# Kernel optimization log

Hardware: AMD Instinct MI355X
Metric: run time of the kernel (lower is better)

## Reference

```python
import jax, jax.numpy as jnp
import numpy as np

INPUT_DIM = 1024
OUTPUT_DIM = 1024
DEGREE = 8


def pentanacci_basis(x, degree):
    # x: [B, I] (already sigmoided). Returns [B, I, degree+1].
    # P0 = 0, P1 = 1, P2 = x, P3 = x, P4 = x^2,
    # Pn = x*P(n-1) + P(n-2) + P(n-3) + P(n-4) + P(n-5) for n >= 5
    zeros = jnp.zeros_like(x)
    ones = jnp.ones_like(x)
    seeds = [zeros, ones, x, x, x * x]
    basis = seeds[: degree + 1]
    for n in range(5, degree + 1):
        basis.append(x * basis[n - 1] + basis[n - 2] + basis[n - 3]
                     + basis[n - 4] + basis[n - 5])
    return jnp.stack(basis, axis=-1)


def setup_inputs() -> dict:
    key = jax.random.key(0)
    kx, kw = jax.random.split(key)
    x = jax.random.normal(kx, (4096, INPUT_DIM), dtype=jnp.float32)
    std = 1.0 / (INPUT_DIM * (DEGREE + 1))
    coeffs = std * jax.random.normal(kw, (INPUT_DIM, OUTPUT_DIM, DEGREE + 1),
                                     dtype=jnp.float32)
    return {"x": x, "coeffs": coeffs}


def reference(x, coeffs):
    degree = coeffs.shape[-1] - 1
    xs = jax.nn.sigmoid(x)                      # [B, I]
    basis = pentanacci_basis(xs, degree)        # [B, I, D+1]
    y = jnp.einsum('bid,iod->bo', basis, coeffs)  # [B, O]
    return y
```

## Files before the change

kernel.cpp:

```cpp
#include <hip/hip_runtime.h>
#include <stdint.h>

#define M_DIM 4096
#define I_DIM 1024
#define O_DIM 1024
#define KB 6
#define K_DIM (I_DIM * KB)
#define SPLITS 4

typedef __attribute__((ext_vector_type(8))) short short8;
typedef __attribute__((ext_vector_type(4))) float f32x4;
typedef __attribute__((ext_vector_type(4))) unsigned int u32x4;
typedef __attribute__((ext_vector_type(4))) float hfloat4;
typedef __attribute__((ext_vector_type(8))) _Float16 h16x8;

__device__ __forceinline__ unsigned short f2bf(float f) {
  union { float f; unsigned int u; } v; v.f = f;
  unsigned int u = v.u;
  unsigned int r = (u + 0x7FFFu + ((u >> 16) & 1u)) >> 16;
  return (unsigned short)r;
}

__global__ __launch_bounds__(256) void k_prep(const float* __restrict__ x,
                                              const float* __restrict__ C,
                                              unsigned short* __restrict__ A,
                                              unsigned short* __restrict__ Bt,
                                              float* __restrict__ partB) {
  const int bid = blockIdx.x;
  if (bid < 2048) {
    int t = bid * 256 + threadIdx.x;
    long e0 = (long)t * 8;
    const hfloat4* xp = (const hfloat4*)(x + e0);
    hfloat4 v0 = xp[0], v1 = xp[1];
    float xv[8];
    xv[0]=v0[0]; xv[1]=v0[1]; xv[2]=v0[2]; xv[3]=v0[3];
    xv[4]=v1[0]; xv[5]=v1[1]; xv[6]=v1[2]; xv[7]=v1[3];
    unsigned short outv[48];
#pragma unroll
    for (int e = 0; e < 8; ++e) {
      float s  = 1.0f / (1.0f + __expf(-xv[e]));
      float b2 = s, b3 = s, b4 = s * s;
      float b5 = fmaf(s, b4, b3 + b2 + 1.0f);
      float b6 = fmaf(s, b5, b4 + b3 + b2 + 1.0f);
      float b7 = fmaf(s, b6, b5 + b4 + b3 + b2);
      float b8 = fmaf(s, b7, b6 + b5 + b4 + b3);
      outv[e*6+0] = f2bf(s);
      outv[e*6+1] = f2bf(b4);
      outv[e*6+2] = f2bf(b5);
      outv[e*6+3] = f2bf(b6);
      outv[e*6+4] = f2bf(b7);
      outv[e*6+5] = f2bf(b8);
    }
    u32x4* dst = (u32x4*)(A + e0 * KB);
    const u32x4* srcv = (const u32x4*)outv;
#pragma unroll
    for (int q = 0; q < 6; ++q) dst[q] = srcv[q];
  } else {
    __shared__ unsigned short tile[32 * 192];
    __shared__ float bred[256];
    int b = bid - 2048;
    int i0 = (b & 31) * 32, o0 = (b >> 5) * 32;
    int t = threadIdx.x;
    int ol = t & 31, ig = t >> 5;
    float bsum = 0.f;
#pragma unroll
    for (int r = 0; r < 4; ++r) {
      int il = ig + r * 8;
      const float* p = C + (size_t)(i0 + il) * (O_DIM * 9) + (size_t)(o0 + ol) * 9;
      float c1 = p[1];
      float c2 = p[2], c3 = p[3], c4 = p[4], c5 = p[5], c6 = p[6], c7 = p[7], c8 = p[8];
      bsum += c1;
      unsigned short* q = &tile[ol * 192 + il * 6];
      q[0] = f2bf(c2 + c3);
      q[1] = f2bf(c4);
      q[2] = f2bf(c5);
      q[3] = f2bf(c6);
      q[4] = f2bf(c7);
      q[5] = f2bf(c8);
    }
    bred[t] = bsum;
    __syncthreads();
    if (t < 32) {
      float s = 0.f;
#pragma unroll
      for (int g = 0; g < 8; ++g) s += bred[g * 32 + t];
      partB[(size_t)(b & 31) * O_DIM + o0 + t] = s;
    }
    const u32x4* lsrc = (const u32x4*)tile;
#pragma unroll
    for (int r = 0; r < 3; ++r) {
      int c = t + r * 256;
      int row = c / 24, off = c % 24;
      u32x4* gdst = (u32x4*)(Bt + (size_t)(o0 + row) * K_DIM + (size_t)i0 * 6 + off * 8);
      *gdst = lsrc[c];
    }
  }
}

__global__ __launch_bounds__(256) void k_bias2(const float* __restrict__ partB,
                                               float* __restrict__ bias) {
  int o = blockIdx.x * 256 + threadIdx.x;
  float s = 0.f;
#pragma unroll
  for (int ib = 0; ib < 32; ++ib) s += partB[(size_t)ib * O_DIM + o];
  bias[o] = s;
}

#define SBAR __builtin_amdgcn_sched_barrier(0)

template<bool SPLIT>
__global__ __launch_bounds__(512, 2) void k_gemm8(const unsigned short* __restrict__ A,
                                                  const unsigned short* __restrict__ B,
                                                  const float* __restrict__ bias,
                                                  void* __restrict__ dst) {
  constexpr int CK = SPLIT ? (K_DIM / SPLITS) : K_DIM;
  constexpr int NT = CK / 64;
  constexpr int PPX = SPLIT ? 8 : 2;
  __shared__ char lds[131072];
  const int tid = threadIdx.x;
  const int lane = tid & 63, wid = tid >> 6;
  const int wm = wid >> 2, wn = wid & 3;
  const int l15 = lane & 15, lk = lane >> 4, l7 = lane & 7;
  const int flat = blockIdx.x + (blockIdx.y << 2) + (blockIdx.z << 6);
  const int xcd = flat & 7, slot = flat >> 3;
  const int panel = xcd * PPX + (slot >> 2);
  const int xn = slot & 3;
  const int ym = panel & 15, zk = panel >> 4;
  const int m0 = ym * 256, n0 = xn * 256;
  const size_t kb = (size_t)zk * CK;
  const int srow = tid >> 3;
  const int cg8 = (((tid & 7) ^ ((tid >> 3) & 7)) * 8);
  const int cx0 = (lk ^ l7) * 16;
  const int cx1 = ((4 + lk) ^ l7) * 16;
  const int arow = wm * 128 + l15;
  const int brow = wn * 64 + l15;

  auto gload = [&](const unsigned short* s, int ldsoff) {
    __builtin_amdgcn_global_load_lds((const __attribute__((address_space(1))) void*)s,
        (__attribute__((address_space(3))) void*)(lds + ldsoff), 16, 0, 0);
  };
  auto stageA = [&](int buf, int h, int kt2) {
    const unsigned short* s = A + (size_t)(m0 + h * 128 + srow) * K_DIM + kb + (size_t)kt2 * 64 + cg8;
    int d = buf * 65536 + h * 16384 + tid * 16;
    gload(s, d);
    gload(s + (size_t)64 * K_DIM, d + 8192);
  };
  auto stageB = [&](int buf, int h, int kt2) {
    const unsigned short* s = B + (size_t)(n0 + h * 128 + srow) * K_DIM + kb + (size_t)kt2 * 64 + cg8;
    int d = buf * 65536 + 32768 + h * 16384 + tid * 16;
    gload(s, d);
    gload(s + (size_t)64 * K_DIM, d + 8192);
  };

  short8 a0[8], b0v[4], a1[8], b1v[4];
  f32x4 acc[8][4];
#pragma unroll
  for (int i = 0; i < 8; ++i)
#pragma unroll
    for (int n = 0; n < 4; ++n)
#pragma unroll
      for (int j = 0; j < 4; ++j) acc[i][n][j] = 0.f;

  auto readK = [&](int buf, int cx, short8 (&av)[8], short8 (&bv)[4]) {
#pragma unroll
    for (int mi = 0; mi < 8; ++mi)
      av[mi] = *(const short8*)(lds + buf * 65536 + (arow + mi * 16) * 128 + cx);
#pragma unroll
    for (int ni = 0; ni < 4; ++ni)
      bv[ni] = *(const short8*)(lds + buf * 65536 + 32768 + (brow + ni * 16) * 128 + cx);
  };
  auto quadK = [&](short8 (&av)[8], short8 (&bv)[4]) {
#pragma unroll
    for (int mi = 0; mi < 8; ++mi)
#pragma unroll
      for (int ni = 0; ni < 4; ++ni)
        acc[mi][ni] = __builtin_amdgcn_mfma_f32_16x16x32_bf16(av[mi], bv[ni], acc[mi][ni], 0, 0, 0);
  };

  stageA(0, 0, 0); stageA(0, 1, 0); stageB(0, 0, 0); stageB(0, 1, 0);
  asm volatile("s_waitcnt vmcnt(0)" ::: "memory"); SBAR;
  __builtin_amdgcn_s_barrier(); SBAR;
  readK(0, cx0, a0, b0v);

#pragma unroll 1
  for (int kt = 0; kt < NT; ++kt) {
    const int buf = kt & 1, nb = buf ^ 1;
    if (kt + 1 < NT) {
      stageA(nb, 0, kt + 1); stageA(nb, 1, kt + 1);
      stageB(nb, 0, kt + 1); stageB(nb, 1, kt + 1);
    }
    readK(buf, cx1, a1, b1v);
    __builtin_amdgcn_s_setprio(1);
    quadK(a0, b0v);
    __builtin_amdgcn_s_setprio(0); SBAR;
    asm volatile("s_waitcnt lgkmcnt(0)" ::: "memory"); SBAR;
    if (kt + 1 < NT) {
      asm volatile("s_waitcnt vmcnt(0)" ::: "memory"); SBAR;
      __builtin_amdgcn_s_barrier(); SBAR;
      readK(nb, cx0, a0, b0v);
    }
    __builtin_amdgcn_s_setprio(1);
    quadK(a1, b1v);
    __builtin_amdgcn_s_setprio(0); SBAR;
  }

  if (SPLIT) {
    _Float16* base = (_Float16*)dst + (size_t)zk * ((size_t)M_DIM * O_DIM);
#pragma unroll
    for (int mi = 0; mi < 8; ++mi) {
      int r0 = m0 + wm * 128 + mi * 16 + (lk << 2);
#pragma unroll
      for (int ni = 0; ni < 4; ++ni) {
        int col = n0 + wn * 64 + ni * 16 + l15;
#pragma unroll
        for (int j = 0; j < 4; ++j)
          base[(size_t)(r0 + j) * O_DIM + col] = (_Float16)acc[mi][ni][j];
      }
    }
  } else {
    float* base = (float*)dst;
#pragma unroll
    for (int mi = 0; mi < 8; ++mi) {
      int r0 = m0 + wm * 128 + mi * 16 + (lk << 2);
#pragma unroll
      for (int ni = 0; ni < 4; ++ni) {
        int col = n0 + wn * 64 + ni * 16 + l15;
        float bv = bias[col];
#pragma unroll
        for (int j = 0; j < 4; ++j)
          base[(size_t)(r0 + j) * O_DIM + col] = acc[mi][ni][j] + bv;
      }
    }
  }
}

__global__ __launch_bounds__(256) void k_reduce(const _Float16* __restrict__ part,
                                                const float* __restrict__ bias,
                                                float* __restrict__ out) {
  size_t t = (size_t)blockIdx.x * 256 + threadIdx.x;
  size_t idx = t * 8;
  const size_t P = (size_t)M_DIM * O_DIM;
  h16x8 s0 = *(const h16x8*)(part + idx);
  h16x8 s1 = *(const h16x8*)(part + P + idx);
  h16x8 s2 = *(const h16x8*)(part + 2 * P + idx);
  h16x8 s3 = *(const h16x8*)(part + 3 * P + idx);
  size_t bo = idx & (O_DIM - 1);
  f32x4 b0 = *(const f32x4*)(bias + bo);
  f32x4 b1 = *(const f32x4*)(bias + bo + 4);
  f32x4 r0, r1;
#pragma unroll
  for (int j = 0; j < 4; ++j) {
    r0[j] = (((float)s0[j] + (float)s1[j]) + ((float)s2[j] + (float)s3[j])) + b0[j];
    r1[j] = (((float)s0[j+4] + (float)s1[j+4]) + ((float)s2[j+4] + (float)s3[j+4])) + b1[j];
  }
  *(f32x4*)(out + idx) = r0;
  *(f32x4*)(out + idx + 4) = r1;
}

extern "C" void kernel_launch(void* const* d_in, const int* in_sizes, int n_in,
                              void* d_out, int out_size, void* d_ws, size_t ws_size,
                              hipStream_t stream) {
  const float* x      = (const float*)d_in[0];
  const float* coeffs = (const float*)d_in[1];
  float* out = (float*)d_out;
  char* ws = (char*)d_ws;
  const size_t offA     = 0;
  const size_t offB     = 50331648;
  const size_t offBias  = offB + 12582912;
  const size_t offPartB = offBias + 4096;
  const size_t offPart  = offPartB + 131072;
  const size_t needSplit = offPart + (size_t)SPLITS * M_DIM * O_DIM * 2;

  unsigned short* A  = (unsigned short*)(ws + offA);
  unsigned short* Bt = (unsigned short*)(ws + offB);
  float* bias        = (float*)(ws + offBias);
  float* partB       = (float*)(ws + offPartB);
  _Float16* part     = (_Float16*)(ws + offPart);

  k_prep<<<3072, 256, 0, stream>>>(x, coeffs, A, Bt, partB);
  k_bias2<<<4, 256, 0, stream>>>(partB, bias);

  if (ws_size >= needSplit) {
    k_gemm8<true><<<dim3(O_DIM / 256, M_DIM / 256, SPLITS), 512, 0, stream>>>(A, Bt, bias, (void*)part);
    k_reduce<<<(M_DIM * O_DIM) / (256 * 8), 256, 0, stream>>>(part, bias, out);
  } else {
    k_gemm8<false><<<dim3(O_DIM / 256, M_DIM / 256, 1), 512, 0, stream>>>(A, Bt, bias, (void*)out);
  }
}
```

Baseline: 86.94 us.

## Store split-K partials in row-quad layout and move both MFMA halves before barrier

The split-K epilogue now writes each lane's four accumulator rows as one packed 8-byte fp16 vector in a row-group-interleaved layout, replacing four scattered 2-byte stores. The reduce kernel reads that layout, adds bias, and transposes through shared memory to write coalesced fp32 rows. The main loop also issues the second MFMA batch before the barrier instead of after it, changing how compute overlaps with the next tile's LDS reads. This adds an LDS round trip and a __syncthreads to the reduce kernel, and shifts the compute/barrier overlap schedule.

```diff
diff --git a/kernel.cpp b/kernel.cpp
--- a/kernel.cpp
+++ b/kernel.cpp
@@ -13,6 +13,7 @@
 typedef __attribute__((ext_vector_type(4))) unsigned int u32x4;
 typedef __attribute__((ext_vector_type(4))) float hfloat4;
 typedef __attribute__((ext_vector_type(8))) _Float16 h16x8;
+typedef __attribute__((ext_vector_type(4))) _Float16 h16x4;
 
 __device__ __forceinline__ unsigned short f2bf(float f) {
   union { float f; unsigned int u; } v; v.f = f;
@@ -112,7 +113,8 @@
 __global__ __launch_bounds__(512, 2) void k_gemm8(const unsigned short* __restrict__ A,
                                                   const unsigned short* __restrict__ B,
                                                   const float* __restrict__ bias,
-                                                  void* __restrict__ dst) {
+                                                  _Float16* __restrict__ part,
+                                                  float* __restrict__ out) {
   constexpr int CK = SPLIT ? (K_DIM / SPLITS) : K_DIM;
   constexpr int NT = CK / 64;
   constexpr int PPX = SPLIT ? 8 : 2;
@@ -192,6 +194,7 @@
     readK(buf, cx1, a1, b1v);
     __builtin_amdgcn_s_setprio(1);
     quadK(a0, b0v);
+    quadK(a1, b1v);
     __builtin_amdgcn_s_setprio(0); SBAR;
     asm volatile("s_waitcnt lgkmcnt(0)" ::: "memory"); SBAR;
     if (kt + 1 < NT) {
@@ -199,26 +202,24 @@
       __builtin_amdgcn_s_barrier(); SBAR;
       readK(nb, cx0, a0, b0v);
     }
-    __builtin_amdgcn_s_setprio(1);
-    quadK(a1, b1v);
-    __builtin_amdgcn_s_setprio(0); SBAR;
   }
 
   if (SPLIT) {
-    _Float16* base = (_Float16*)dst + (size_t)zk * ((size_t)M_DIM * O_DIM);
+    _Float16* base = part + (size_t)zk * ((size_t)M_DIM * O_DIM);
+    const int gb0 = (m0 >> 2) + wm * 32 + lk;
 #pragma unroll
     for (int mi = 0; mi < 8; ++mi) {
-      int r0 = m0 + wm * 128 + mi * 16 + (lk << 2);
+      int g = gb0 + mi * 4;
 #pragma unroll
       for (int ni = 0; ni < 4; ++ni) {
         int col = n0 + wn * 64 + ni * 16 + l15;
-#pragma unroll
-        for (int j = 0; j < 4; ++j)
-          base[(size_t)(r0 + j) * O_DIM + col] = (_Float16)acc[mi][ni][j];
+        h16x4 v;
+#pragma unroll
+        for (int j = 0; j < 4; ++j) v[j] = (_Float16)acc[mi][ni][j];
+        *(h16x4*)(base + ((size_t)g * O_DIM + col) * 4) = v;
       }
     }
   } else {
-    float* base = (float*)dst;
 #pragma unroll
     for (int mi = 0; mi < 8; ++mi) {
       int r0 = m0 + wm * 128 + mi * 16 + (lk << 2);
@@ -228,7 +229,7 @@
         float bv = bias[col];
 #pragma unroll
         for (int j = 0; j < 4; ++j)
-          base[(size_t)(r0 + j) * O_DIM + col] = acc[mi][ni][j] + bv;
+          out[(size_t)(r0 + j) * O_DIM + col] = acc[mi][ni][j] + bv;
       }
     }
   }
@@ -237,24 +238,31 @@
 __global__ __launch_bounds__(256) void k_reduce(const _Float16* __restrict__ part,
                                                 const float* __restrict__ bias,
                                                 float* __restrict__ out) {
-  size_t t = (size_t)blockIdx.x * 256 + threadIdx.x;
-  size_t idx = t * 8;
+  __shared__ float lt[4][512];
+  const int b = blockIdx.x, tt = threadIdx.x;
   const size_t P = (size_t)M_DIM * O_DIM;
+  size_t idx = (size_t)b * 2048 + (size_t)tt * 8;
   h16x8 s0 = *(const h16x8*)(part + idx);
   h16x8 s1 = *(const h16x8*)(part + P + idx);
   h16x8 s2 = *(const h16x8*)(part + 2 * P + idx);
   h16x8 s3 = *(const h16x8*)(part + 3 * P + idx);
-  size_t bo = idx & (O_DIM - 1);
-  f32x4 b0 = *(const f32x4*)(bias + bo);
-  f32x4 b1 = *(const f32x4*)(bias + bo + 4);
-  f32x4 r0, r1;
-#pragma unroll
-  for (int j = 0; j < 4; ++j) {
-    r0[j] = (((float)s0[j] + (float)s1[j]) + ((float)s2[j] + (float)s3[j])) + b0[j];
-    r1[j] = (((float)s0[j+4] + (float)s1[j+4]) + ((float)s2[j+4] + (float)s3[j+4])) + b1[j];
-  }
-  *(f32x4*)(out + idx) = r0;
-  *(f32x4*)(out + idx + 4) = r1;
+  const int g = b >> 1;
+  const int cbase = (b & 1) << 9;
+  const int c0 = tt * 2;
+  float bv0 = bias[cbase + c0], bv1 = bias[cbase + c0 + 1];
+#pragma unroll
+  for (int k = 0; k < 8; ++k) {
+    float r = (((float)s0[k] + (float)s1[k]) + ((float)s2[k] + (float)s3[k]))
+              + ((k < 4) ? bv0 : bv1);
+    lt[k & 3][c0 + (k >> 2)] = r;
+  }
+  __syncthreads();
+  const int rj = tt >> 6, lc = (tt & 63) * 8;
+  f32x4 v0 = *(const f32x4*)&lt[rj][lc];
+  f32x4 v1 = *(const f32x4*)&lt[rj][lc + 4];
+  float* o = out + (size_t)(4 * g + rj) * O_DIM + cbase + lc;
+  *(f32x4*)o = v0;
+  *(f32x4*)(o + 4) = v1;
 }
 
 extern "C" void kernel_launch(void* const* d_in, const int* in_sizes, int n_in,
@@ -281,9 +289,9 @@
   k_bias2<<<4, 256, 0, stream>>>(partB, bias);
 
   if (ws_size >= needSplit) {
-    k_gemm8<true><<<dim3(O_DIM / 256, M_DIM / 256, SPLITS), 512, 0, stream>>>(A, Bt, bias, (void*)part);
+    k_gemm8<true><<<dim3(4, 16, SPLITS), 512, 0, stream>>>(A, Bt, bias, part, out);
     k_reduce<<<(M_DIM * O_DIM) / (256 * 8), 256, 0, stream>>>(part, bias, out);
   } else {
-    k_gemm8<false><<<dim3(O_DIM / 256, M_DIM / 256, 1), 512, 0, stream>>>(A, Bt, bias, (void*)out);
-  }
-}
+    k_gemm8<false><<<dim3(4, 16, 1), 512, 0, stream>>>(A, Bt, bias, part, out);
+  }
+}
```

New measurement: 86.21 us, median of 3. About the same (-0.8%).
